# Performance work log

Measured on AMD Instinct MI355X. Metric: run time of the kernel, lower is better.

## Reference

```python
import jax, jax.numpy as jnp
import numpy as np

B, S, D, H = 2, 2048, 768, 12
DH = D // H  # 64

def setup_inputs() -> dict:
    key = jax.random.key(0)
    ks = jax.random.split(key, 5)
    x = jax.random.normal(ks[0], (B, S, D), dtype=jnp.float32)
    # causal mask: True = attend (lower triangular), bool -> constant w.r.t. grads
    attn_mask = jnp.tril(jnp.ones((S, S), dtype=bool))[None, None, :, :]
    c_attn_w = jax.random.normal(ks[1], (D, 3 * D), dtype=jnp.float32) * 0.02
    c_attn_b = jnp.zeros((3 * D,), dtype=jnp.float32)
    c_proj_w = jax.random.normal(ks[2], (D, D), dtype=jnp.float32) * 0.02
    c_proj_b = jnp.zeros((D,), dtype=jnp.float32)
    return {"x": x, "attn_mask": attn_mask, "c_attn_w": c_attn_w,
            "c_attn_b": c_attn_b, "c_proj_w": c_proj_w, "c_proj_b": c_proj_b}

def reference(x, attn_mask, c_attn_w, c_attn_b, c_proj_w, c_proj_b):
    # qkv projection (Conv1D == addmm)
    qkv = x @ c_attn_w + c_attn_b                      # [B,S,3D]
    q, k, v = jnp.split(qkv, 3, axis=-1)               # each [B,S,D]
    def split_heads(t):
        return t.reshape(B, S, H, DH).transpose(0, 2, 1, 3)  # [B,H,S,DH]
    q, k, v = split_heads(q), split_heads(k), split_heads(v)
    scores = jnp.einsum('bhqd,bhkd->bhqk', q, k) / jnp.sqrt(jnp.float32(DH))
    neg = jnp.asarray(-1e9, dtype=scores.dtype)
    scores = jnp.where(attn_mask, scores, neg)         # additive causal mask
    probs = jax.nn.softmax(scores, axis=-1)            # dropout: eval mode (identity)
    out = jnp.einsum('bhqk,bhkd->bhqd', probs, v)      # [B,H,S,DH]
    out = out.transpose(0, 2, 1, 3).reshape(B, S, D)   # merge heads
    return out @ c_proj_w + c_proj_b
```

## Files before the change

kernel.cpp:

```cpp
#include <hip/hip_runtime.h>
#include <cstddef>
#include <cstdint>

#define Bsz  2
#define Ssz  2048
#define Dsz  768
#define Hsz  12
#define DHsz 64
#define Msz  4096
#define N3sz 2304
#define Kdim 768

typedef short bf16x8 __attribute__((ext_vector_type(8)));
typedef float f32x4  __attribute__((ext_vector_type(4)));
typedef const __attribute__((address_space(1))) void gvoid;
typedef __attribute__((address_space(3))) void lvoid;

static __device__ __forceinline__ unsigned short f2bf(float f) {
    unsigned int u = __builtin_bit_cast(unsigned int, f);
    u += 0x7FFFu + ((u >> 16) & 1u);
    return (unsigned short)(u >> 16);
}
static __device__ __forceinline__ unsigned int pk2bf(float a, float b) {
    return (unsigned int)f2bf(a) | ((unsigned int)f2bf(b) << 16);
}

__global__ __launch_bounds__(256) void cast_x_kernel(
    const float* __restrict__ X, unsigned short* __restrict__ Xb)
{
    const size_t i = ((size_t)blockIdx.x * 256 + threadIdx.x) * 8;
    const float4 a = *(const float4*)&X[i];
    const float4 b = *(const float4*)&X[i + 4];
    ushort4 lo, hi;
    lo.x = f2bf(a.x); lo.y = f2bf(a.y); lo.z = f2bf(a.z); lo.w = f2bf(a.w);
    hi.x = f2bf(b.x); hi.y = f2bf(b.y); hi.z = f2bf(b.z); hi.w = f2bf(b.w);
    *(ushort4*)&Xb[i] = lo;
    *(ushort4*)&Xb[i + 4] = hi;
}

__global__ __launch_bounds__(256) void transpose_cast_kernel(
    const float* __restrict__ W, unsigned short* __restrict__ Wt, int N)
{
    __shared__ float T[64][65];
    const int tid = threadIdx.x;
    const int n0 = blockIdx.x << 6;
    const int k0 = blockIdx.y << 6;
#pragma unroll
    for (int p = 0; p < 4; ++p) {
        const int idx = p * 256 + tid;
        const int r  = idx >> 4;
        const int c4 = (idx & 15) << 2;
        const float4 v = *(const float4*)&W[(size_t)(k0 + r) * N + n0 + c4];
        T[r][c4 + 0] = v.x; T[r][c4 + 1] = v.y;
        T[r][c4 + 2] = v.z; T[r][c4 + 3] = v.w;
    }
    __syncthreads();
#pragma unroll
    for (int p = 0; p < 4; ++p) {
        const int idx = p * 256 + tid;
        const int r  = idx >> 4;
        const int c4 = (idx & 15) << 2;
        ushort4 o;
        o.x = f2bf(T[c4 + 0][r]); o.y = f2bf(T[c4 + 1][r]);
        o.z = f2bf(T[c4 + 2][r]); o.w = f2bf(T[c4 + 3][r]);
        *(ushort4*)&Wt[(size_t)(n0 + r) * Kdim + k0 + c4] = o;
    }
}

template<bool QKV>
__global__ __launch_bounds__(256) void gemm_mfma_kernel(
    const unsigned short* __restrict__ A,
    const unsigned short* __restrict__ Bt,
    const float* __restrict__ bias,
    unsigned short* __restrict__ Qo, unsigned short* __restrict__ Ko,
    unsigned short* __restrict__ Vo, float* __restrict__ Out)
{
    __shared__ unsigned short Als[128 * 64];
    __shared__ unsigned short Bls[128 * 64];

    const int tid  = threadIdx.x;
    const int w    = tid >> 6;
    const int lane = tid & 63;
    const int quad = lane >> 4;
    const int t16  = lane & 15;
    const int wm   = w & 1;
    const int wn   = w >> 1;
    const int m0   = blockIdx.y << 7;
    const int n0   = blockIdx.x << 7;

    const int lrow = lane >> 3;
    const int lch  = lane & 7;
    const unsigned short* Ag = A  + (size_t)(m0 + lrow) * Kdim + ((lch ^ lrow) << 3);
    const unsigned short* Bg = Bt + (size_t)(n0 + lrow) * Kdim + ((lch ^ lrow) << 3);

    f32x4 acc[4][4];
#pragma unroll
    for (int mt = 0; mt < 4; ++mt)
#pragma unroll
        for (int nt = 0; nt < 4; ++nt) acc[mt][nt] = (f32x4)(0.f);

    for (int k0 = 0; k0 < Kdim; k0 += 64) {
        __syncthreads();
#pragma unroll
        for (int t = 0; t < 4; ++t) {
            const int i = (w << 2) + t;
            __builtin_amdgcn_global_load_lds(
                (gvoid*)(Ag + (size_t)(i << 3) * Kdim + k0),
                (lvoid*)(Als + (i << 9)), 16, 0, 0);
            __builtin_amdgcn_global_load_lds(
                (gvoid*)(Bg + (size_t)(i << 3) * Kdim + k0),
                (lvoid*)(Bls + (i << 9)), 16, 0, 0);
        }
        __syncthreads();

#pragma unroll
        for (int ks = 0; ks < 2; ++ks) {
            const int sl = (((ks << 2) + quad) ^ (t16 & 7)) << 3;
            bf16x8 af[4], bfr[4];
#pragma unroll
            for (int mt = 0; mt < 4; ++mt)
                af[mt] = *(const bf16x8*)&Als[(((wm << 6) + (mt << 4) + t16) << 6) + sl];
#pragma unroll
            for (int nt = 0; nt < 4; ++nt)
                bfr[nt] = *(const bf16x8*)&Bls[(((wn << 6) + (nt << 4) + t16) << 6) + sl];
#pragma unroll
            for (int mt = 0; mt < 4; ++mt)
#pragma unroll
                for (int nt = 0; nt < 4; ++nt)
                    acc[mt][nt] = __builtin_amdgcn_mfma_f32_16x16x32_bf16(
                        af[mt], bfr[nt], acc[mt][nt], 0, 0, 0);
        }
    }

    if (QKV) {
#pragma unroll
        for (int nt = 0; nt < 4; ++nt) {
            const int n   = n0 + (wn << 6) + (nt << 4) + t16;
            const int seg = n / Dsz;
            const int d0  = n % Dsz;
            const int h   = d0 >> 6;
            const int d   = d0 & 63;
            unsigned short* dst = (seg == 0) ? Qo : (seg == 1) ? Ko : Vo;
            const float sc = (seg == 0) ? 0.18033688f : 1.0f;
            const float bn = bias[n];
#pragma unroll
            for (int mt = 0; mt < 4; ++mt) {
                const int mb = m0 + (wm << 6) + (mt << 4) + (quad << 2);
#pragma unroll
                for (int r = 0; r < 4; ++r) {
                    const int m  = mb + r;
                    const int bI = m >> 11;
                    const int s  = m & 2047;
                    dst[(((size_t)bI * Hsz + h) * Ssz + s) * DHsz + d] =
                        f2bf((acc[mt][nt][r] + bn) * sc);
                }
            }
        }
    } else {
#pragma unroll
        for (int nt = 0; nt < 4; ++nt) {
            const int n  = n0 + (wn << 6) + (nt << 4) + t16;
            const float bn = bias[n];
#pragma unroll
            for (int mt = 0; mt < 4; ++mt) {
                const int mb = m0 + (wm << 6) + (mt << 4) + (quad << 2);
#pragma unroll
                for (int r = 0; r < 4; ++r)
                    Out[(size_t)(mb + r) * Dsz + n] = acc[mt][nt][r] + bn;
            }
        }
    }
}

__global__ __launch_bounds__(256) void attn_mfma_kernel(
    const unsigned short* __restrict__ Q, const unsigned short* __restrict__ K,
    const unsigned short* __restrict__ V, unsigned short* __restrict__ Aout)
{
    __shared__ unsigned short Kls[64 * 72];
    __shared__ unsigned short Vls[64 * 72];
    __shared__ unsigned short Pls[4][16 * 72];

    const int tid  = threadIdx.x;
    const int w    = tid >> 6;
    const int lane = tid & 63;
    const int quad = lane >> 4;
    const int t16  = lane & 15;

    const int qt   = 31 - (blockIdx.x / 24);
    const int bh   = blockIdx.x % 24;
    const int q0   = qt << 6;
    const int bIdx = bh / Hsz;
    const int h    = bh % Hsz;

    const size_t base = (size_t)bh * Ssz * DHsz;

    const int kv_a = tid >> 3;
    const int kc_a = tid & 7;
    const int kvp  = tid & 31;
    const int dc   = tid >> 5;

    bf16x8 qf[2];
#pragma unroll
    for (int s = 0; s < 2; ++s)
        qf[s] = *(const bf16x8*)&Q[base + (size_t)(q0 + w * 16 + t16) * DHsz
                                   + s * 32 + quad * 8];

    f32x4 O[4];
    float m_i = -1e30f, l_i = 0.f;
#pragma unroll
    for (int dt = 0; dt < 4; ++dt) O[dt] = (f32x4)(0.f);

    uint4 kr0, kr1, va, vb;
    {
        const unsigned short* Kb = K + base;
        const unsigned short* Vb = V + base;
        kr0 = *(const uint4*)&Kb[(size_t)kv_a * DHsz + kc_a * 8];
        kr1 = *(const uint4*)&Kb[(size_t)(kv_a + 32) * DHsz + kc_a * 8];
        va  = *(const uint4*)&Vb[(size_t)(2 * kvp) * DHsz + dc * 8];
        vb  = *(const uint4*)&Vb[(size_t)(2 * kvp + 1) * DHsz + dc * 8];
    }

    for (int kt = 0; kt <= qt; ++kt) {
        __syncthreads();

        *(uint4*)&Kls[kv_a * 72 + kc_a * 8] = kr0;
        *(uint4*)&Kls[(kv_a + 32) * 72 + kc_a * 8] = kr1;
        {
            const unsigned short* pa = reinterpret_cast<const unsigned short*>(&va);
            const unsigned short* pb = reinterpret_cast<const unsigned short*>(&vb);
#pragma unroll
            for (int j = 0; j < 8; ++j) {
                const unsigned int pk = (unsigned int)pa[j] | ((unsigned int)pb[j] << 16);
                *(unsigned int*)&Vls[(dc * 8 + j) * 72 + 2 * kvp] = pk;
            }
        }
        __syncthreads();

        if (kt < qt) {
            const unsigned short* Kb = K + base + (size_t)((kt + 1) << 6) * DHsz;
            const unsigned short* Vb = V + base + (size_t)((kt + 1) << 6) * DHsz;
            kr0 = *(const uint4*)&Kb[(size_t)kv_a * DHsz + kc_a * 8];
            kr1 = *(const uint4*)&Kb[(size_t)(kv_a + 32) * DHsz + kc_a * 8];
            va  = *(const uint4*)&Vb[(size_t)(2 * kvp) * DHsz + dc * 8];
            vb  = *(const uint4*)&Vb[(size_t)(2 * kvp + 1) * DHsz + dc * 8];
        }

        f32x4 St[4];
#pragma unroll
        for (int kb = 0; kb < 4; ++kb) St[kb] = (f32x4)(0.f);
#pragma unroll
        for (int s = 0; s < 2; ++s)
#pragma unroll
            for (int kb = 0; kb < 4; ++kb) {
                const bf16x8 kf = *(const bf16x8*)&Kls[(kb * 16 + t16) * 72
                                                       + s * 32 + quad * 8];
                St[kb] = __builtin_amdgcn_mfma_f32_16x16x32_bf16(kf, qf[s], St[kb], 0, 0, 0);
            }

        if (kt == qt) {
            const int qrel = w * 16 + t16;
#pragma unroll
            for (int kb = 0; kb < 4; ++kb) {
                const int kvb = kb * 16 + quad * 4;
#pragma unroll
                for (int r = 0; r < 4; ++r)
                    if (kvb + r > qrel) St[kb][r] = -1e30f;
            }
        }

        float pm = St[0][0];
#pragma unroll
        for (int kb = 0; kb < 4; ++kb)
#pragma unroll
            for (int r = 0; r < 4; ++r) pm = fmaxf(pm, St[kb][r]);
        pm = fmaxf(pm, __shfl_xor(pm, 16));
        pm = fmaxf(pm, __shfl_xor(pm, 32));
        const float mn = fmaxf(m_i, pm);
        const float alpha = exp2f(m_i - mn);
        m_i = mn;

        float ps = 0.f;
#pragma unroll
        for (int kb = 0; kb < 4; ++kb) {
            float p0 = exp2f(St[kb][0] - mn);
            float p1 = exp2f(St[kb][1] - mn);
            float p2 = exp2f(St[kb][2] - mn);
            float p3 = exp2f(St[kb][3] - mn);
            ps += (p0 + p1) + (p2 + p3);
            uint2 pk;
            pk.x = pk2bf(p0, p1);
            pk.y = pk2bf(p2, p3);
            *(uint2*)&Pls[w][t16 * 72 + kb * 16 + quad * 4] = pk;
        }
        ps += __shfl_xor(ps, 16);
        ps += __shfl_xor(ps, 32);
        l_i = l_i * alpha + ps;
#pragma unroll
        for (int dt = 0; dt < 4; ++dt) O[dt] *= alpha;

#pragma unroll
        for (int s = 0; s < 2; ++s) {
            const bf16x8 pf = *(const bf16x8*)&Pls[w][t16 * 72 + s * 32 + quad * 8];
#pragma unroll
            for (int dt = 0; dt < 4; ++dt) {
                const bf16x8 vf = *(const bf16x8*)&Vls[(dt * 16 + t16) * 72
                                                       + s * 32 + quad * 8];
                O[dt] = __builtin_amdgcn_mfma_f32_16x16x32_bf16(vf, pf, O[dt], 0, 0, 0);
            }
        }
    }

    {
        const float inv = 1.0f / l_i;
        const int q = q0 + w * 16 + t16;
        unsigned short* dst = Aout + ((size_t)bIdx * Ssz + q) * Dsz + (h << 6);
#pragma unroll
        for (int dt = 0; dt < 4; ++dt) {
            uint2 o;
            o.x = pk2bf(O[dt][0] * inv, O[dt][1] * inv);
            o.y = pk2bf(O[dt][2] * inv, O[dt][3] * inv);
            *(uint2*)&dst[dt * 16 + quad * 4] = o;
        }
    }
}

extern "C" void kernel_launch(void* const* d_in, const int* in_sizes, int n_in,
                              void* d_out, int out_size, void* d_ws, size_t ws_size,
                              hipStream_t stream) {
    const float* x        = (const float*)d_in[0];
    const float* c_attn_w = (const float*)d_in[2];
    const float* c_attn_b = (const float*)d_in[3];
    const float* c_proj_w = (const float*)d_in[4];
    const float* c_proj_b = (const float*)d_in[5];
    float* out = (float*)d_out;

    const size_t T = (size_t)Msz * Dsz;
    unsigned short* xb     = (unsigned short*)d_ws;
    unsigned short* Wqkvt  = xb + T;
    unsigned short* Wprojt = Wqkvt + (size_t)N3sz * Kdim;
    unsigned short* Qw     = Wprojt + (size_t)Dsz * Kdim;
    unsigned short* Kw     = Qw + T;
    unsigned short* Vw     = Kw + T;
    unsigned short* Ab     = Vw + T;

    cast_x_kernel<<<T / 2048, 256, 0, stream>>>(x, xb);
    transpose_cast_kernel<<<dim3(N3sz / 64, Kdim / 64), 256, 0, stream>>>(
        c_attn_w, Wqkvt, N3sz);
    transpose_cast_kernel<<<dim3(Dsz / 64, Kdim / 64), 256, 0, stream>>>(
        c_proj_w, Wprojt, Dsz);

    gemm_mfma_kernel<true><<<dim3(N3sz / 128, Msz / 128), 256, 0, stream>>>(
        xb, Wqkvt, c_attn_b, Qw, Kw, Vw, nullptr);
    attn_mfma_kernel<<<32 * 24, 256, 0, stream>>>(Qw, Kw, Vw, Ab);
    gemm_mfma_kernel<false><<<dim3(Dsz / 128, Msz / 128), 256, 0, stream>>>(
        Ab, Wprojt, c_proj_b, nullptr, nullptr, nullptr, out);
}
```

Measured before the change: 195.6 us.

## Merge prep kernels into one launch and vectorize GEMM epilogue stores

Combines the x cast and both weight transpose-casts into a single prep kernel that dispatches on block index, removing two kernel launches. In the GEMMs it swaps the MFMA operand order so each lane holds four consecutive output columns, which allows vectorized bias loads and packed 8-byte bf16 / 16-byte fp32 stores instead of scattered scalar stores. It also hoists the Q/K/V segment and head computation out of the inner loop.

```diff
diff --git a/kernel.cpp b/kernel.cpp
--- a/kernel.cpp
+++ b/kernel.cpp
@@ -25,26 +25,12 @@
     return (unsigned int)f2bf(a) | ((unsigned int)f2bf(b) << 16);
 }
 
-__global__ __launch_bounds__(256) void cast_x_kernel(
-    const float* __restrict__ X, unsigned short* __restrict__ Xb)
+static __device__ __forceinline__ void transpose_body(
+    const float* __restrict__ W, unsigned short* __restrict__ Wt, int N,
+    int bx, int by, int tid, float (*T)[65])
 {
-    const size_t i = ((size_t)blockIdx.x * 256 + threadIdx.x) * 8;
-    const float4 a = *(const float4*)&X[i];
-    const float4 b = *(const float4*)&X[i + 4];
-    ushort4 lo, hi;
-    lo.x = f2bf(a.x); lo.y = f2bf(a.y); lo.z = f2bf(a.z); lo.w = f2bf(a.w);
-    hi.x = f2bf(b.x); hi.y = f2bf(b.y); hi.z = f2bf(b.z); hi.w = f2bf(b.w);
-    *(ushort4*)&Xb[i] = lo;
-    *(ushort4*)&Xb[i + 4] = hi;
-}
-
-__global__ __launch_bounds__(256) void transpose_cast_kernel(
-    const float* __restrict__ W, unsigned short* __restrict__ Wt, int N)
-{
-    __shared__ float T[64][65];
-    const int tid = threadIdx.x;
-    const int n0 = blockIdx.x << 6;
-    const int k0 = blockIdx.y << 6;
+    const int n0 = bx << 6;
+    const int k0 = by << 6;
 #pragma unroll
     for (int p = 0; p < 4; ++p) {
         const int idx = p * 256 + tid;
@@ -64,6 +50,32 @@
         o.x = f2bf(T[c4 + 0][r]); o.y = f2bf(T[c4 + 1][r]);
         o.z = f2bf(T[c4 + 2][r]); o.w = f2bf(T[c4 + 3][r]);
         *(ushort4*)&Wt[(size_t)(n0 + r) * Kdim + k0 + c4] = o;
+    }
+}
+
+__global__ __launch_bounds__(256) void prep_kernel(
+    const float* __restrict__ X, unsigned short* __restrict__ Xb,
+    const float* __restrict__ Wqkv, unsigned short* __restrict__ Wqkvt,
+    const float* __restrict__ Wproj, unsigned short* __restrict__ Wprojt)
+{
+    __shared__ float T[64][65];
+    const int bid = blockIdx.x;
+    const int tid = threadIdx.x;
+    if (bid < 1536) {
+        const size_t i = ((size_t)bid * 256 + tid) * 8;
+        const float4 a = *(const float4*)&X[i];
+        const float4 b = *(const float4*)&X[i + 4];
+        ushort4 lo, hi;
+        lo.x = f2bf(a.x); lo.y = f2bf(a.y); lo.z = f2bf(a.z); lo.w = f2bf(a.w);
+        hi.x = f2bf(b.x); hi.y = f2bf(b.y); hi.z = f2bf(b.z); hi.w = f2bf(b.w);
+        *(ushort4*)&Xb[i] = lo;
+        *(ushort4*)&Xb[i + 4] = hi;
+    } else if (bid < 1536 + 432) {
+        const int idx = bid - 1536;
+        transpose_body(Wqkv, Wqkvt, N3sz, idx % 36, idx / 36, tid, T);
+    } else {
+        const int idx = bid - 1968;
+        transpose_body(Wproj, Wprojt, Dsz, idx % 12, idx / 12, tid, T);
     }
 }
 
@@ -128,45 +140,48 @@
 #pragma unroll
                 for (int nt = 0; nt < 4; ++nt)
                     acc[mt][nt] = __builtin_amdgcn_mfma_f32_16x16x32_bf16(
-                        af[mt], bfr[nt], acc[mt][nt], 0, 0, 0);
+                        bfr[nt], af[mt], acc[mt][nt], 0, 0, 0);
         }
     }
 
     if (QKV) {
+        const int nb  = n0 + (wn << 6);
+        const int seg = nb / Dsz;
+        unsigned short* dst0 = (seg == 0) ? Qo : (seg == 1) ? Ko : Vo;
+        const float sc = (seg == 0) ? 0.18033688f : 1.0f;
+        const int h = (nb % Dsz) >> 6;
 #pragma unroll
         for (int nt = 0; nt < 4; ++nt) {
-            const int n   = n0 + (wn << 6) + (nt << 4) + t16;
-            const int seg = n / Dsz;
-            const int d0  = n % Dsz;
-            const int h   = d0 >> 6;
-            const int d   = d0 & 63;
-            unsigned short* dst = (seg == 0) ? Qo : (seg == 1) ? Ko : Vo;
-            const float sc = (seg == 0) ? 0.18033688f : 1.0f;
-            const float bn = bias[n];
+            const int n = nb + (nt << 4) + (quad << 2);
+            const int d = (nt << 4) + (quad << 2);
+            const float4 bn = *(const float4*)&bias[n];
 #pragma unroll
             for (int mt = 0; mt < 4; ++mt) {
-                const int mb = m0 + (wm << 6) + (mt << 4) + (quad << 2);
-#pragma unroll
-                for (int r = 0; r < 4; ++r) {
-                    const int m  = mb + r;
-                    const int bI = m >> 11;
-                    const int s  = m & 2047;
-                    dst[(((size_t)bI * Hsz + h) * Ssz + s) * DHsz + d] =
-                        f2bf((acc[mt][nt][r] + bn) * sc);
-                }
+                const int m  = m0 + (wm << 6) + (mt << 4) + t16;
+                const int bI = m >> 11;
+                const int s  = m & 2047;
+                uint2 o;
+                o.x = pk2bf((acc[mt][nt][0] + bn.x) * sc,
+                            (acc[mt][nt][1] + bn.y) * sc);
+                o.y = pk2bf((acc[mt][nt][2] + bn.z) * sc,
+                            (acc[mt][nt][3] + bn.w) * sc);
+                *(uint2*)&dst0[(((size_t)bI * Hsz + h) * Ssz + s) * DHsz + d] = o;
             }
         }
     } else {
 #pragma unroll
         for (int nt = 0; nt < 4; ++nt) {
-            const int n  = n0 + (wn << 6) + (nt << 4) + t16;
-            const float bn = bias[n];
+            const int n = n0 + (wn << 6) + (nt << 4) + (quad << 2);
+            const float4 bn = *(const float4*)&bias[n];
 #pragma unroll
             for (int mt = 0; mt < 4; ++mt) {
-                const int mb = m0 + (wm << 6) + (mt << 4) + (quad << 2);
-#pragma unroll
-                for (int r = 0; r < 4; ++r)
-                    Out[(size_t)(mb + r) * Dsz + n] = acc[mt][nt][r] + bn;
+                const int m = m0 + (wm << 6) + (mt << 4) + t16;
+                float4 o;
+                o.x = acc[mt][nt][0] + bn.x;
+                o.y = acc[mt][nt][1] + bn.y;
+                o.z = acc[mt][nt][2] + bn.z;
+                o.w = acc[mt][nt][3] + bn.w;
+                *(float4*)&Out[(size_t)m * Dsz + n] = o;
             }
         }
     }
@@ -343,12 +358,7 @@
     unsigned short* Vw     = Kw + T;
     unsigned short* Ab     = Vw + T;
 
-    cast_x_kernel<<<T / 2048, 256, 0, stream>>>(x, xb);
-    transpose_cast_kernel<<<dim3(N3sz / 64, Kdim / 64), 256, 0, stream>>>(
-        c_attn_w, Wqkvt, N3sz);
-    transpose_cast_kernel<<<dim3(Dsz / 64, Kdim / 64), 256, 0, stream>>>(
-        c_proj_w, Wprojt, Dsz);
-
+    prep_kernel<<<2112, 256, 0, stream>>>(x, xb, c_attn_w, Wqkvt, c_proj_w, Wprojt);
     gemm_mfma_kernel<true><<<dim3(N3sz / 128, Msz / 128), 256, 0, stream>>>(
         xb, Wqkvt, c_attn_b, Qw, Kw, Vw, nullptr);
     attn_mfma_kernel<<<32 * 24, 256, 0, stream>>>(Qw, Kw, Vw, Ab);
```

Result: faster. 185.0 us (-5.4%).
